# Kernel optimization log

Hardware: AMD Instinct MI355X
Metric: run time of the kernel (lower is better)

The kernel has to match this reference:

```python
import jax, jax.numpy as jnp
import numpy as np

# dims: V vocab, D embed, C classes, S seq, L layers, M proj_dim (random features), B batch
V, D, C, S, L, M, B = 32000, 512, 2, 2048, 4, 64, 16
H = 4 * D  # FFN hidden


def setup_inputs() -> dict:
    key = jax.random.key(0)
    ks = jax.random.split(key, 16)
    sc = 0.02
    n = lambda k, shape, s=sc: jax.random.normal(k, shape, jnp.float32) * s
    return {
        'x': jax.random.randint(ks[0], (B, S), 0, V),
        'embed': n(ks[1], (V, D)),
        'pos': n(ks[2], (S, D)),
        'Wq': n(ks[3], (L, D, D)), 'bq': jnp.zeros((L, D), jnp.float32),
        'Wk': n(ks[4], (L, D, D)), 'bk': jnp.zeros((L, D), jnp.float32),
        'Wv': n(ks[5], (L, D, D)), 'bv': jnp.zeros((L, D), jnp.float32),
        'P': jax.random.normal(ks[6], (L, D, M), jnp.float32) / np.sqrt(D),  # Performer random-feature projection
        'Wo': n(ks[7], (L, D, D)), 'bo': jnp.zeros((L, D), jnp.float32),
        'ln_g': jnp.ones((L, D), jnp.float32), 'ln_b': jnp.zeros((L, D), jnp.float32),
        'W1': n(ks[8], (L, D, H)), 'b1': jnp.zeros((L, H), jnp.float32),
        'W2': n(ks[9], (L, H, D)), 'b2': jnp.zeros((L, D), jnp.float32),
        'Wc1': n(ks[10], (D, D // 2)), 'bc1': jnp.zeros((D // 2,), jnp.float32),
        'Wc2': n(ks[11], (D // 2, C)), 'bc2': jnp.zeros((C,), jnp.float32),
    }


def _layernorm(x, g, b, eps=1e-5):
    mu = x.mean(-1, keepdims=True)
    var = ((x - mu) ** 2).mean(-1, keepdims=True)
    return (x - mu) * jax.lax.rsqrt(var + eps) * g + b


def reference(x, embed, pos, Wq, bq, Wk, bk, Wv, bv, P, Wo, bo,
              ln_g, ln_b, W1, b1, W2, b2, Wc1, bc1, Wc2, bc2):
    # token embedding + learned positional embedding
    h = embed[x] + pos[None, :, :]  # [B,S,D]
    for l in range(L):
        r = h
        # Performer linear attention
        q = h @ Wq[l] + bq[l]
        k = h @ Wk[l] + bk[l]
        v = h @ Wv[l] + bv[l]
        pq = jax.nn.elu(q @ P[l]) + 1.0  # [B,S,M] positive feature map
        pk = jax.nn.elu(k @ P[l]) + 1.0
        kv = jnp.einsum('bsm,bsd->bmd', pk, v)              # associative K^T V reduction
        z = jnp.einsum('bsm,bm->bs', pq, pk.sum(axis=1)) + 1e-6
        att = jnp.einsum('bsm,bmd->bsd', pq, kv) / z[..., None]
        att = att @ Wo[l] + bo[l]
        # LayerNorm -> FFN (dropout is identity in eval)
        hn = _layernorm(att, ln_g[l], ln_b[l])
        ff = jax.nn.gelu(hn @ W1[l] + b1[l], approximate=False) @ W2[l] + b2[l]
        h = ff + r  # residual around the whole Sequential block
    pooled = h[:, 0, :]  # CLS pooling
    hid = jax.nn.relu(pooled @ Wc1 + bc1)
    return hid @ Wc2 + bc2  # [B,C] logits
```

## Files before the change

kernel.cpp:

```cpp
#include <hip/hip_runtime.h>
#include <hip/hip_bf16.h>
#include <math.h>

constexpr int kV = 32000;
constexpr int kD = 512;
constexpr int kC = 2;
constexpr int kS = 2048;
constexpr int kL = 4;
constexpr int kM = 64;
constexpr int kB = 16;
constexpr int kH = 2048;
constexpr int kBS = kB * kS;

typedef __hip_bfloat16 bf16;
using bf16x8 = __attribute__((ext_vector_type(8))) short;
using f32x4  = __attribute__((ext_vector_type(4))) float;

#define GLOBAL_LOAD_LDS16(gp, lp)                                              \
  __builtin_amdgcn_global_load_lds(                                            \
      (const __attribute__((address_space(1))) void*)(gp),                     \
      (__attribute__((address_space(3))) void*)(lp), 16, 0, 0)

__device__ inline unsigned short f2bf_u16(float f) {
  bf16 b = __float2bfloat16(f);
  return *reinterpret_cast<unsigned short*>(&b);
}

__global__ __launch_bounds__(256) void embed_kernel(const int* __restrict__ x,
    const float* __restrict__ emb, const float* __restrict__ pos,
    float* __restrict__ h, bf16* __restrict__ hb) {
  int tid = blockIdx.x * 256 + threadIdx.x;
  int row = tid >> 7;
  int d4  = tid & 127;
  int tok = x[row];
  int s   = row & (kS - 1);
  float4 e = ((const float4*)emb)[(size_t)tok * 128 + d4];
  float4 p = ((const float4*)pos)[(size_t)s * 128 + d4];
  float4 o;
  o.x = e.x + p.x; o.y = e.y + p.y; o.z = e.z + p.z; o.w = e.w + p.w;
  ((float4*)h)[(size_t)row * 128 + d4] = o;
  ushort4 ub;
  ub.x = f2bf_u16(o.x); ub.y = f2bf_u16(o.y);
  ub.z = f2bf_u16(o.z); ub.w = f2bf_u16(o.w);
  ((ushort4*)hb)[(size_t)row * 128 + d4] = ub;
}

__global__ __launch_bounds__(256) void transpose_cast_kernel(
    const float* __restrict__ W, bf16* __restrict__ Wt, int K, int N) {
  __shared__ float tile[32][33];
  const int k0 = blockIdx.x * 32, n0 = blockIdx.y * 32;
  int tx = threadIdx.x & 31, ty = threadIdx.x >> 5;
#pragma unroll
  for (int i = 0; i < 32; i += 8)
    tile[ty + i][tx] = W[(size_t)(k0 + ty + i) * N + n0 + tx];
  __syncthreads();
#pragma unroll
  for (int i = 0; i < 32; i += 8)
    Wt[(size_t)(n0 + ty + i) * K + k0 + tx] = __float2bfloat16(tile[tx][ty + i]);
}

__global__ __launch_bounds__(256) void cast_bf16_kernel(
    const float* __restrict__ src, bf16* __restrict__ dst) {
  int gid = blockIdx.x * 256 + threadIdx.x;
  float4 v = ((const float4*)src)[gid];
  ushort4 u;
  u.x = f2bf_u16(v.x); u.y = f2bf_u16(v.y);
  u.z = f2bf_u16(v.z); u.w = f2bf_u16(v.w);
  ((ushort4*)dst)[gid] = u;
}

__global__ __launch_bounds__(256) void zero512_kernel(float* __restrict__ p) {
  if (threadIdx.x < 128) ((float4*)p)[threadIdx.x] = make_float4(0.f, 0.f, 0.f, 0.f);
}

__global__ __launch_bounds__(256) void wfold_dual_kernel(
    const float* __restrict__ Wq, const float* __restrict__ Wk,
    const float* __restrict__ P, bf16* __restrict__ Wqpt,
    bf16* __restrict__ Wkpt) {
  int gid = blockIdx.x * 256 + threadIdx.x;
  const float* W = (gid < 32768) ? Wq : Wk;
  bf16* out      = (gid < 32768) ? Wqpt : Wkpt;
  int id = gid & 32767;
  int m  = id & 63;
  int kk = id >> 6;
  float a0 = 0.f, a1 = 0.f, a2 = 0.f, a3 = 0.f;
#pragma unroll 4
  for (int c = 0; c < kD; c += 4) {
    float4 w = *(const float4*)&W[(size_t)kk * kD + c];
    a0 = fmaf(w.x, P[(size_t)(c + 0) * kM + m], a0);
    a1 = fmaf(w.y, P[(size_t)(c + 1) * kM + m], a1);
    a2 = fmaf(w.z, P[(size_t)(c + 2) * kM + m], a2);
    a3 = fmaf(w.w, P[(size_t)(c + 3) * kM + m], a3);
  }
  out[(size_t)m * kD + kk] = __float2bfloat16((a0 + a1) + (a2 + a3));
}

__global__ __launch_bounds__(128) void bfold_kernel(const float* __restrict__ bq,
    const float* __restrict__ bk, const float* __restrict__ P,
    float* __restrict__ bqp, float* __restrict__ bkp) {
  int m = threadIdx.x & (kM - 1);
  const float* src = (threadIdx.x >> 6) ? bk : bq;
  float* dst = (threadIdx.x >> 6) ? bkp : bqp;
  float acc = 0.f;
  for (int c = 0; c < kD; ++c) acc += src[c] * P[(size_t)c * kM + m];
  dst[m] = acc;
}

__global__ __launch_bounds__(256) void bvwo_kernel(const float* __restrict__ bv,
    const float* __restrict__ Wo, float* __restrict__ bvWo) {
  __shared__ float part[4][64];
  int d0 = blockIdx.x * 64;
  int dc = threadIdx.x & 63;
  int eg = threadIdx.x >> 6;
  float acc = 0.f;
  int e0 = eg * 128;
#pragma unroll 4
  for (int e = e0; e < e0 + 128; ++e)
    acc = fmaf(bv[e], Wo[(size_t)e * kD + d0 + dc], acc);
  part[eg][dc] = acc;
  __syncthreads();
  if (eg == 0)
    bvWo[d0 + dc] = (part[0][dc] + part[1][dc]) + (part[2][dc] + part[3][dc]);
}

template <int BK, int BN, int ACT, bool HAS_RES, bool HAS_OUTER, bool WRITE_F32, bool WRITE_BF16>
__global__ __launch_bounds__(256) void mfma_gemm(
    const bf16* __restrict__ A, const bf16* __restrict__ Wt,
    const float* __restrict__ bias, const float* __restrict__ rowv,
    const float* __restrict__ colv, const float* __restrict__ res,
    float* __restrict__ C, bf16* __restrict__ Cb, int K, int N) {
  constexpr int NJ = BN / 32;
  constexpr int CPR = BK / 8;
  constexpr int SW = (BK == 32) ? 1 : 0;
  __shared__ short As[128 * BK];
  __shared__ short Bs[BN * BK];
  const int tid  = threadIdx.x;
  const int lane = tid & 63;
  const int wave = tid >> 6;
  const int nx = gridDim.x;
  const int SH = (gridDim.y & 7) ? gridDim.y : 8;
  const int b_lin = blockIdx.y * nx + blockIdx.x;
  const int stripe = b_lin / (nx * SH);
  const int rem = b_lin - stripe * (nx * SH);
  const int row0 = (stripe * SH + (rem % SH)) * 128;
  const int col0 = (rem / SH) * BN;
  const int wr = (wave & 1) * 64;
  const int wc = (wave >> 1) * (BN / 2);
  const int lcol = lane & 15;
  const int quad = lane >> 4;

  f32x4 acc[4][NJ];
#pragma unroll
  for (int i = 0; i < 4; ++i)
#pragma unroll
    for (int j = 0; j < NJ; ++j) acc[i][j] = (f32x4){0.f, 0.f, 0.f, 0.f};

  for (int k0 = 0; k0 < K; k0 += BK) {
#pragma unroll
    for (int p = 0; p < 128 * CPR / 256; ++p) {
      int idx = p * 256 + tid;
      int r = idx / CPR;
      int kc = (idx % CPR) ^ ((r >> SW) & (CPR - 1));
      GLOBAL_LOAD_LDS16(&A[(size_t)(row0 + r) * K + k0 + kc * 8], &As[idx * 8]);
    }
#pragma unroll
    for (int p = 0; p < BN * CPR / 256; ++p) {
      int idx = p * 256 + tid;
      int r = idx / CPR;
      int kc = (idx % CPR) ^ ((r >> SW) & (CPR - 1));
      GLOBAL_LOAD_LDS16(&Wt[(size_t)(col0 + r) * K + k0 + kc * 8], &Bs[idx * 8]);
    }
    __syncthreads();
#pragma unroll
    for (int kh = 0; kh < BK / 32; ++kh) {
      bf16x8 af[4], bfr[NJ];
#pragma unroll
      for (int i = 0; i < 4; ++i) {
        int rr = wr + i * 16 + lcol;
        int slot = (kh * 4 + quad) ^ ((rr >> SW) & (CPR - 1));
        af[i] = *(const bf16x8*)&As[(rr * CPR + slot) * 8];
      }
#pragma unroll
      for (int j = 0; j < NJ; ++j) {
        int rr = wc + j * 16 + lcol;
        int slot = (kh * 4 + quad) ^ ((rr >> SW) & (CPR - 1));
        bfr[j] = *(const bf16x8*)&Bs[(rr * CPR + slot) * 8];
      }
#pragma unroll
      for (int i = 0; i < 4; ++i)
#pragma unroll
        for (int j = 0; j < NJ; ++j)
          acc[i][j] = __builtin_amdgcn_mfma_f32_16x16x32_bf16(af[i], bfr[j], acc[i][j], 0, 0, 0);
    }
    __syncthreads();
  }

#pragma unroll
  for (int i = 0; i < 4; ++i) {
#pragma unroll
    for (int r = 0; r < 4; ++r) {
      int grow = row0 + wr + i * 16 + quad * 4 + r;
#pragma unroll
      for (int j = 0; j < NJ; ++j) {
        int gcol = col0 + wc + j * 16 + lcol;
        float v = acc[i][j][r];
        if (HAS_OUTER) v += rowv[grow] * colv[gcol];
        else v += bias[gcol];
        if (ACT == 2) v = 0.5f * v * (1.0f + erff(v * 0.70710678118654752f));
        size_t off = (size_t)grow * N + gcol;
        if (HAS_RES) v += res[off];
        if (WRITE_F32) C[off] = v;
        if (WRITE_BF16) Cb[off] = __float2bfloat16(v);
      }
    }
  }
}

template <int ACT, bool HAS_RES, bool WRITE_F32, bool WRITE_BF16>
__global__ __launch_bounds__(512) void mfma_gemm_256(
    const bf16* __restrict__ A, const bf16* __restrict__ Wt,
    const float* __restrict__ bias, const float* __restrict__ res,
    float* __restrict__ C, bf16* __restrict__ Cb, int K, int N) {
  constexpr int BK = 64, BN = 128, BM = 256;
  __shared__ short As[BM * BK];
  __shared__ short Bs[BN * BK];
  const int tid  = threadIdx.x;
  const int lane = tid & 63;
  const int wave = tid >> 6;
  const int nx = gridDim.x;
  const int SH = (gridDim.y & 7) ? gridDim.y : 8;
  const int b_lin = blockIdx.y * nx + blockIdx.x;
  const int stripe = b_lin / (nx * SH);
  const int rem = b_lin - stripe * (nx * SH);
  const int row0 = (stripe * SH + (rem % SH)) * BM;
  const int col0 = (rem / SH) * BN;
  const int wr = (wave & 3) * 64;
  const int wc = (wave >> 2) * 64;
  const int lcol = lane & 15;
  const int quad = lane >> 4;

  f32x4 acc[4][4];
#pragma unroll
  for (int i = 0; i < 4; ++i)
#pragma unroll
    for (int j = 0; j < 4; ++j) acc[i][j] = (f32x4){0.f, 0.f, 0.f, 0.f};

  for (int k0 = 0; k0 < K; k0 += BK) {
#pragma unroll
    for (int p = 0; p < 4; ++p) {
      int idx = p * 512 + tid;
      int r = idx >> 3;
      int kc = (idx & 7) ^ (r & 7);
      GLOBAL_LOAD_LDS16(&A[(size_t)(row0 + r) * K + k0 + kc * 8], &As[idx * 8]);
    }
#pragma unroll
    for (int p = 0; p < 2; ++p) {
      int idx = p * 512 + tid;
      int r = idx >> 3;
      int kc = (idx & 7) ^ (r & 7);
      GLOBAL_LOAD_LDS16(&Wt[(size_t)(col0 + r) * K + k0 + kc * 8], &Bs[idx * 8]);
    }
    __syncthreads();
#pragma unroll
    for (int kh = 0; kh < 2; ++kh) {
      bf16x8 af[4], bfr[4];
#pragma unroll
      for (int i = 0; i < 4; ++i) {
        int rr = wr + i * 16 + lcol;
        int slot = (kh * 4 + quad) ^ (rr & 7);
        af[i] = *(const bf16x8*)&As[(rr * 8 + slot) * 8];
      }
#pragma unroll
      for (int j = 0; j < 4; ++j) {
        int rr = wc + j * 16 + lcol;
        int slot = (kh * 4 + quad) ^ (rr & 7);
        bfr[j] = *(const bf16x8*)&Bs[(rr * 8 + slot) * 8];
      }
#pragma unroll
      for (int i = 0; i < 4; ++i)
#pragma unroll
        for (int j = 0; j < 4; ++j)
          acc[i][j] = __builtin_amdgcn_mfma_f32_16x16x32_bf16(af[i], bfr[j], acc[i][j], 0, 0, 0);
    }
    __syncthreads();
  }

#pragma unroll
  for (int i = 0; i < 4; ++i) {
#pragma unroll
    for (int r = 0; r < 4; ++r) {
      int grow = row0 + wr + i * 16 + quad * 4 + r;
#pragma unroll
      for (int j = 0; j < 4; ++j) {
        int gcol = col0 + wc + j * 16 + lcol;
        float v = acc[i][j][r] + bias[gcol];
        if (ACT == 2) v = 0.5f * v * (1.0f + erff(v * 0.70710678118654752f));
        size_t off = (size_t)grow * N + gcol;
        if (HAS_RES) v += res[off];
        if (WRITE_F32) C[off] = v;
        if (WRITE_BF16) Cb[off] = __float2bfloat16(v);
      }
    }
  }
}

__global__ __launch_bounds__(256) void skinny_dual_gemm(
    const bf16* __restrict__ A, const bf16* __restrict__ Wq,
    const bf16* __restrict__ Wk, const float* __restrict__ bq,
    const float* __restrict__ bk, float* __restrict__ pq,
    float* __restrict__ pk) {
  __shared__ short As[64 * 32];
  __shared__ short Bs[128 * 32];
  const int tid  = threadIdx.x;
  const int lane = tid & 63;
  const int wave = tid >> 6;
  const int row0 = blockIdx.x * 64;
  const int lcol = lane & 15;
  const int quad = lane >> 4;

  f32x4 accq[4], acck[4];
#pragma unroll
  for (int i = 0; i < 4; ++i) {
    accq[i] = (f32x4){0.f, 0.f, 0.f, 0.f};
    acck[i] = (f32x4){0.f, 0.f, 0.f, 0.f};
  }

  for (int k0 = 0; k0 < kD; k0 += 32) {
    {
      int r = tid >> 2;
      int kc = (tid & 3) ^ ((r >> 1) & 3);
      GLOBAL_LOAD_LDS16(&A[(size_t)(row0 + r) * kD + k0 + kc * 8], &As[tid * 8]);
    }
#pragma unroll
    for (int p = 0; p < 2; ++p) {
      int idx = p * 256 + tid;
      int r = idx >> 2;
      int kc = (idx & 3) ^ ((r >> 1) & 3);
      const bf16* src = (r < 64) ? &Wq[(size_t)r * kD + k0 + kc * 8]
                                 : &Wk[(size_t)(r - 64) * kD + k0 + kc * 8];
      GLOBAL_LOAD_LDS16(src, &Bs[idx * 8]);
    }
    __syncthreads();
    bf16x8 af[4], bq_f, bk_f;
#pragma unroll
    for (int i = 0; i < 4; ++i) {
      int rr = i * 16 + lcol;
      af[i] = *(const bf16x8*)&As[(rr * 4 + (quad ^ ((rr >> 1) & 3))) * 8];
    }
    {
      int rr = wave * 16 + lcol;
      bq_f = *(const bf16x8*)&Bs[(rr * 4 + (quad ^ ((rr >> 1) & 3))) * 8];
      int rr2 = 64 + wave * 16 + lcol;
      bk_f = *(const bf16x8*)&Bs[(rr2 * 4 + (quad ^ ((rr2 >> 1) & 3))) * 8];
    }
#pragma unroll
    for (int i = 0; i < 4; ++i) {
      accq[i] = __builtin_amdgcn_mfma_f32_16x16x32_bf16(af[i], bq_f, accq[i], 0, 0, 0);
      acck[i] = __builtin_amdgcn_mfma_f32_16x16x32_bf16(af[i], bk_f, acck[i], 0, 0, 0);
    }
    __syncthreads();
  }

#pragma unroll
  for (int i = 0; i < 4; ++i) {
#pragma unroll
    for (int r = 0; r < 4; ++r) {
      int grow = row0 + i * 16 + quad * 4 + r;
      int gcol = wave * 16 + lcol;
      float vq = accq[i][r] + bq[gcol];
      vq = (vq > 0.f) ? (vq + 1.f) : expf(vq);
      pq[(size_t)grow * kM + gcol] = vq;
      float vk = acck[i][r] + bk[gcol];
      vk = (vk > 0.f) ? (vk + 1.f) : expf(vk);
      pk[(size_t)grow * kM + gcol] = vk;
    }
  }
}

__global__ __launch_bounds__(256) void kvh_split_kernel(const float* __restrict__ pk,
    const bf16* __restrict__ hb, float* __restrict__ part) {
  __shared__ float pkS[16][64];
  __shared__ float vS[16][256];
  const int d0 = blockIdx.x * 256, b = blockIdx.y, split = blockIdx.z;
  const int s_beg = split * 128;
  const float* pkb = pk + (size_t)b * kS * kM;
  const bf16* hbb  = hb + (size_t)b * kS * kD;
  const int tid = threadIdx.x;
  const int tx = tid & 15, ty = tid >> 4;
  float4 acc[4][4];
#pragma unroll
  for (int i = 0; i < 4; ++i)
#pragma unroll
    for (int j = 0; j < 4; ++j) acc[i][j] = make_float4(0.f, 0.f, 0.f, 0.f);

  for (int s0 = s_beg; s0 < s_beg + 128; s0 += 16) {
    {
      int e = tid * 4;
      int sr = e >> 6, mc = e & 63;
      *(float4*)&pkS[sr][mc] = *(const float4*)&pkb[(size_t)(s0 + sr) * kM + mc];
    }
#pragma unroll
    for (int p = 0; p < 2; ++p) {
      int idx = p * 256 + tid;
      int sr = idx >> 5, dc8 = idx & 31;
      uint4 raw = *(const uint4*)&hbb[(size_t)(s0 + sr) * kD + d0 + dc8 * 8];
      float4 f0, f1;
      f0.x = __uint_as_float(raw.x << 16);
      f0.y = __uint_as_float(raw.x & 0xffff0000u);
      f0.z = __uint_as_float(raw.y << 16);
      f0.w = __uint_as_float(raw.y & 0xffff0000u);
      f1.x = __uint_as_float(raw.z << 16);
      f1.y = __uint_as_float(raw.z & 0xffff0000u);
      f1.z = __uint_as_float(raw.w << 16);
      f1.w = __uint_as_float(raw.w & 0xffff0000u);
      *(float4*)&vS[sr][dc8 * 8]     = f0;
      *(float4*)&vS[sr][dc8 * 8 + 4] = f1;
    }
    __syncthreads();
#pragma unroll
    for (int sr = 0; sr < 16; ++sr) {
      float a[4];
#pragma unroll
      for (int i = 0; i < 4; ++i) a[i] = pkS[sr][ty * 4 + i];
      float4 bv4[4];
#pragma unroll
      for (int j = 0; j < 4; ++j) bv4[j] = *(const float4*)&vS[sr][tx * 16 + j * 4];
#pragma unroll
      for (int i = 0; i < 4; ++i)
#pragma unroll
        for (int j = 0; j < 4; ++j) {
          acc[i][j].x += a[i] * bv4[j].x;
          acc[i][j].y += a[i] * bv4[j].y;
          acc[i][j].z += a[i] * bv4[j].z;
          acc[i][j].w += a[i] * bv4[j].w;
        }
    }
    __syncthreads();
  }
  float* pp = part + (((size_t)split * kB + b) * kM) * kD;
#pragma unroll
  for (int i = 0; i < 4; ++i)
#pragma unroll
    for (int j = 0; j < 4; ++j)
      *(float4*)&pp[(size_t)(ty * 4 + i) * kD + d0 + tx * 16 + j * 4] = acc[i][j];
}

__global__ __launch_bounds__(256) void kvh_reduce_kernel(const float* __restrict__ part,
                                                         bf16* __restrict__ kvhb) {
  int gid = blockIdx.x * 256 + threadIdx.x;
  float4 s = make_float4(0.f, 0.f, 0.f, 0.f);
#pragma unroll
  for (int sp = 0; sp < 16; ++sp) {
    float4 p = ((const float4*)part)[(size_t)sp * (kB * kM * kD / 4) + gid];
    s.x += p.x; s.y += p.y; s.z += p.z; s.w += p.w;
  }
  ushort4 u;
  u.x = f2bf_u16(s.x); u.y = f2bf_u16(s.y);
  u.z = f2bf_u16(s.z); u.w = f2bf_u16(s.w);
  ((ushort4*)kvhb)[gid] = u;
}

__global__ __launch_bounds__(256) void zero_pks_kernel(float* __restrict__ p) {
  ((float4*)p)[threadIdx.x] = make_float4(0.f, 0.f, 0.f, 0.f);
}

__global__ __launch_bounds__(256) void pksum_kernel(const float* __restrict__ pk,
                                                    float* __restrict__ pksum) {
  __shared__ float part[4][64];
  int b = blockIdx.x >> 4;
  int split = blockIdx.x & 15;
  int lane = threadIdx.x & 63, w = threadIdx.x >> 6;
  float s = 0.f;
  int base = split * 128 + w * 32;
  for (int i = 0; i < 32; ++i)
    s += pk[((size_t)b * kS + base + i) * kM + lane];
  part[w][lane] = s;
  __syncthreads();
  if (w == 0)
    atomicAdd(&pksum[b * kM + lane],
              part[0][lane] + part[1][lane] + part[2][lane] + part[3][lane]);
}

__global__ __launch_bounds__(256) void z_kernel(const float* __restrict__ pq,
    const float* __restrict__ pksum, float* __restrict__ z) {
  int row = blockIdx.x * 4 + (threadIdx.x >> 6);
  int lane = threadIdx.x & 63;
  int b = row >> 11;
  float v = pq[(size_t)row * kM + lane] * pksum[b * kM + lane];
#pragma unroll
  for (int off = 32; off; off >>= 1) v += __shfl_down(v, off);
  if (lane == 0) z[row] = v + 1e-6f;
}

__global__ __launch_bounds__(256) void att_ln_kernel(
    const float* __restrict__ pq, const float* __restrict__ kvo,
    const float* __restrict__ z, const float* __restrict__ bo,
    const float* __restrict__ g, const float* __restrict__ bb,
    bf16* __restrict__ out) {
  __shared__ float pqS[32][68];
  __shared__ float kvS[16][520];
  const int s0 = blockIdx.x * 32, b = blockIdx.y;
  const int tid = threadIdx.x;
  const int tx = tid & 15, ty = tid >> 4;

#pragma unroll
  for (int i = 0; i < 2; ++i) {
    int f4 = tid + i * 256;
    int r = f4 >> 4, c = (f4 & 15) * 4;
    *(float4*)&pqS[r][c] = *(const float4*)&pq[((size_t)(b * kS + s0 + r)) * kM + c];
  }

  float4 acc[2][8];
#pragma unroll
  for (int i = 0; i < 2; ++i)
#pragma unroll
    for (int j = 0; j < 8; ++j) acc[i][j] = make_float4(0.f, 0.f, 0.f, 0.f);

  for (int m0 = 0; m0 < kM; m0 += 16) {
#pragma unroll
    for (int p = 0; p < 8; ++p) {
      int idx = p * 256 + tid;
      int sr = idx >> 7, c4 = idx & 127;
      *(float4*)&kvS[sr][c4 * 4] =
          *(const float4*)&kvo[((size_t)b * kM + m0 + sr) * kD + c4 * 4];
    }
    __syncthreads();
#pragma unroll
    for (int mm = 0; mm < 16; ++mm) {
      float a0 = pqS[ty * 2 + 0][m0 + mm];
      float a1 = pqS[ty * 2 + 1][m0 + mm];
#pragma unroll
      for (int j = 0; j < 8; ++j) {
        float4 bv = *(const float4*)&kvS[mm][j * 64 + tx * 4];
        acc[0][j].x += a0 * bv.x; acc[0][j].y += a0 * bv.y;
        acc[0][j].z += a0 * bv.z; acc[0][j].w += a0 * bv.w;
        acc[1][j].x += a1 * bv.x; acc[1][j].y += a1 * bv.y;
        acc[1][j].z += a1 * bv.z; acc[1][j].w += a1 * bv.w;
      }
    }
    __syncthreads();
  }

  float zi0 = 1.0f / z[b * kS + s0 + ty * 2 + 0];
  float zi1 = 1.0f / z[b * kS + s0 + ty * 2 + 1];
#pragma unroll
  for (int j = 0; j < 8; ++j) {
    float4 bo4 = *(const float4*)&bo[j * 64 + tx * 4];
    acc[0][j].x = acc[0][j].x * zi0 + bo4.x; acc[0][j].y = acc[0][j].y * zi0 + bo4.y;
    acc[0][j].z = acc[0][j].z * zi0 + bo4.z; acc[0][j].w = acc[0][j].w * zi0 + bo4.w;
    acc[1][j].x = acc[1][j].x * zi1 + bo4.x; acc[1][j].y = acc[1][j].y * zi1 + bo4.y;
    acc[1][j].z = acc[1][j].z * zi1 + bo4.z; acc[1][j].w = acc[1][j].w * zi1 + bo4.w;
  }

#pragma unroll
  for (int i = 0; i < 2; ++i) {
    float s = 0.f;
#pragma unroll
    for (int j = 0; j < 8; ++j)
      s += (acc[i][j].x + acc[i][j].y) + (acc[i][j].z + acc[i][j].w);
    s += __shfl_xor(s, 1); s += __shfl_xor(s, 2);
    s += __shfl_xor(s, 4); s += __shfl_xor(s, 8);
    float mean = s * (1.0f / kD);
    float v2 = 0.f;
#pragma unroll
    for (int j = 0; j < 8; ++j) {
      float dx = acc[i][j].x - mean, dy = acc[i][j].y - mean;
      float dz = acc[i][j].z - mean, dw = acc[i][j].w - mean;
      v2 += (dx * dx + dy * dy) + (dz * dz + dw * dw);
    }
    v2 += __shfl_xor(v2, 1); v2 += __shfl_xor(v2, 2);
    v2 += __shfl_xor(v2, 4); v2 += __shfl_xor(v2, 8);
    float rstd = rsqrtf(v2 * (1.0f / kD) + 1e-5f);
    size_t rowoff = ((size_t)(b * kS + s0 + ty * 2 + i)) * kD;
#pragma unroll
    for (int j = 0; j < 8; ++j) {
      int col = j * 64 + tx * 4;
      float4 g4 = *(const float4*)&g[col];
      float4 b4 = *(const float4*)&bb[col];
      ushort4 u;
      u.x = f2bf_u16((acc[i][j].x - mean) * rstd * g4.x + b4.x);
      u.y = f2bf_u16((acc[i][j].y - mean) * rstd * g4.y + b4.y);
      u.z = f2bf_u16((acc[i][j].z - mean) * rstd * g4.z + b4.z);
      u.w = f2bf_u16((acc[i][j].w - mean) * rstd * g4.w + b4.w);
      *(ushort4*)&out[rowoff + col] = u;
    }
  }
}

__global__ __launch_bounds__(256) void cls_kernel(const float* __restrict__ h,
    const float* __restrict__ Wc1, const float* __restrict__ bc1,
    const float* __restrict__ Wc2, const float* __restrict__ bc2,
    float* __restrict__ out) {
  __shared__ float r0[4], r1[4];
  int b = blockIdx.x;
  int j = threadIdx.x;
  const float* p = h + (size_t)b * kS * kD;
  float acc = bc1[j];
  for (int i = 0; i < kD; ++i) acc += p[i] * Wc1[i * (kD / 2) + j];
  acc = fmaxf(acc, 0.f);
  float p0 = acc * Wc2[j * kC + 0];
  float p1 = acc * Wc2[j * kC + 1];
#pragma unroll
  for (int off = 32; off; off >>= 1) {
    p0 += __shfl_down(p0, off);
    p1 += __shfl_down(p1, off);
  }
  if ((j & 63) == 0) { r0[j >> 6] = p0; r1[j >> 6] = p1; }
  __syncthreads();
  if (j == 0) {
    out[b * kC + 0] = r0[0] + r0[1] + r0[2] + r0[3] + bc2[0];
    out[b * kC + 1] = r1[0] + r1[1] + r1[2] + r1[3] + bc2[1];
  }
}

extern "C" void kernel_launch(void* const* d_in, const int* in_sizes, int n_in,
                              void* d_out, int out_size, void* d_ws, size_t ws_size,
                              hipStream_t stream) {
  const int*   x    = (const int*)  d_in[0];
  const float* emb  = (const float*)d_in[1];
  const float* pos  = (const float*)d_in[2];
  const float* Wq   = (const float*)d_in[3];
  const float* bq   = (const float*)d_in[4];
  const float* Wk   = (const float*)d_in[5];
  const float* bk   = (const float*)d_in[6];
  const float* Wv   = (const float*)d_in[7];
  const float* bv   = (const float*)d_in[8];
  const float* P    = (const float*)d_in[9];
  const float* Wo   = (const float*)d_in[10];
  const float* bo   = (const float*)d_in[11];
  const float* ln_g = (const float*)d_in[12];
  const float* ln_b = (const float*)d_in[13];
  const float* W1   = (const float*)d_in[14];
  const float* b1   = (const float*)d_in[15];
  const float* W2   = (const float*)d_in[16];
  const float* b2   = (const float*)d_in[17];
  const float* Wc1  = (const float*)d_in[18];
  const float* bc1  = (const float*)d_in[19];
  const float* Wc2  = (const float*)d_in[20];
  const float* bc2  = (const float*)d_in[21];
  float* out = (float*)d_out;

  float* h    = (float*)d_ws;
  float* t0   = h    + (size_t)kBS * kD;
  float* pq   = t0   + (size_t)kBS * kD;
  float* pk   = pq   + (size_t)kBS * kM;
  float* kvo  = pk   + (size_t)kBS * kM;
  float* pks  = kvo  + (size_t)kB * kM * kD;
  float* zb   = pks  + (size_t)kB * kM;
  float* bqp  = zb   + kBS;
  float* bkp  = bqp  + kM;
  float* bvWo = bkp  + kM;
  float* zeros= bvWo + kD;
  bf16* hb    = (bf16*)(zeros + kD);
  bf16* ab    = hb + (size_t)kBS * kD;
  bf16* Wqpt  = ab  + (size_t)kBS * kD;
  bf16* Wkpt  = Wqpt + (size_t)kM * kD;
  bf16* Wot   = Wkpt + (size_t)kM * kD;
  bf16* Wvc   = Wot + (size_t)kD * kD;
  bf16* WvWot = Wvc + (size_t)kD * kD;
  bf16* W1t   = WvWot + (size_t)kD * kD;
  bf16* W2t   = W1t + (size_t)kD * kH;
  bf16* kvhb  = W2t + (size_t)kD * kH;
  bf16* F     = (bf16*)t0;
  float* kvpart = (float*)ab;

  zero512_kernel<<<1, 256, 0, stream>>>(zeros);
  embed_kernel<<<kBS * (kD / 4) / 256, 256, 0, stream>>>(x, emb, pos, h, hb);

  for (int l = 0; l < kL; ++l) {
    const float* Pl = P + (size_t)l * kD * kM;

    wfold_dual_kernel<<<256, 256, 0, stream>>>(
        Wq + (size_t)l * kD * kD, Wk + (size_t)l * kD * kD, Pl, Wqpt, Wkpt);
    bfold_kernel<<<1, 128, 0, stream>>>(bq + l * kD, bk + l * kD, Pl, bqp, bkp);
    transpose_cast_kernel<<<dim3(kD / 32, kD / 32), 256, 0, stream>>>(
        Wo + (size_t)l * kD * kD, Wot, kD, kD);
    cast_bf16_kernel<<<kD * kD / 1024, 256, 0, stream>>>(Wv + (size_t)l * kD * kD, Wvc);
    mfma_gemm<32, 64, 0, false, false, false, true><<<dim3(8, 4), 256, 0, stream>>>(
        Wot, Wvc, zeros, nullptr, nullptr, nullptr, nullptr, WvWot, kD, kD);
    bvwo_kernel<<<8, 256, 0, stream>>>(bv + l * kD, Wo + (size_t)l * kD * kD, bvWo);
    transpose_cast_kernel<<<dim3(kD / 32, kH / 32), 256, 0, stream>>>(
        W1 + (size_t)l * kD * kH, W1t, kD, kH);
    transpose_cast_kernel<<<dim3(kH / 32, kD / 32), 256, 0, stream>>>(
        W2 + (size_t)l * kH * kD, W2t, kH, kD);

    skinny_dual_gemm<<<kBS / 64, 256, 0, stream>>>(hb, Wqpt, Wkpt, bqp, bkp, pq, pk);
    kvh_split_kernel<<<dim3(kD / 256, kB, 16), 256, 0, stream>>>(pk, hb, kvpart);
    kvh_reduce_kernel<<<kB * kM * kD / 1024, 256, 0, stream>>>(kvpart, kvhb);
    zero_pks_kernel<<<1, 256, 0, stream>>>(pks);
    pksum_kernel<<<kB * 16, 256, 0, stream>>>(pk, pks);
    z_kernel<<<kBS / 4, 256, 0, stream>>>(pq, pks, zb);
    mfma_gemm<32, 64, 0, false, true, true, false><<<dim3(8, 8), 256, 0, stream>>>(
        kvhb, WvWot, nullptr, pks, bvWo, nullptr, kvo, nullptr, kD, kD);
    att_ln_kernel<<<dim3(kS / 32, kB), 256, 0, stream>>>(
        pq, kvo, zb, bo + l * kD, ln_g + l * kD, ln_b + l * kD, ab);
    for (int c = 0; c < 2; ++c) {
      size_t ro = (size_t)c * 16384;
      mfma_gemm_256<2, false, false, true><<<dim3(kH / 128, 16384 / 256), 512, 0, stream>>>(
          ab + ro * kD, W1t, b1 + l * kH, nullptr, nullptr, F, kD, kH);
      mfma_gemm_256<0, true, true, true><<<dim3(kD / 128, 16384 / 256), 512, 0, stream>>>(
          F, W2t, b2 + l * kD, h + ro * kD, h + ro * kD, hb + ro * kD, kH, kD);
    }
  }

  cls_kernel<<<kB, 256, 0, stream>>>(h, Wc1, bc1, Wc2, bc2, out);
}
```

Measured before the change: 1.789 ms.

## Double-buffer LDS in FFN GEMM with smaller 128x128 tiles

Rewrites the FFN GEMM kernel to use two LDS buffers so the global-to-LDS loads for the next K tile are issued before computing the current one, with one barrier per iteration instead of two. The block tile shrinks from 256x128 to 128x128, each wave now computing 64x32, and the grid doubles in the M direction. This aims to hide memory latency and raise occupancy, at the cost of less data reuse per block and fewer MFMAs per LDS read.

```diff
diff --git a/kernel.cpp b/kernel.cpp
--- a/kernel.cpp
+++ b/kernel.cpp
@@ -217,13 +217,13 @@
 }
 
 template <int ACT, bool HAS_RES, bool WRITE_F32, bool WRITE_BF16>
-__global__ __launch_bounds__(512) void mfma_gemm_256(
+__global__ __launch_bounds__(512) void mfma_gemm_2ph(
     const bf16* __restrict__ A, const bf16* __restrict__ Wt,
     const float* __restrict__ bias, const float* __restrict__ res,
     float* __restrict__ C, bf16* __restrict__ Cb, int K, int N) {
-  constexpr int BK = 64, BN = 128, BM = 256;
-  __shared__ short As[BM * BK];
-  __shared__ short Bs[BN * BK];
+  constexpr int BK = 64, BN = 128, BM = 128;
+  __shared__ short As[2][BM * BK];
+  __shared__ short Bs[2][BN * BK];
   const int tid  = threadIdx.x;
   const int lane = tid & 63;
   const int wave = tid >> 6;
@@ -234,55 +234,71 @@
   const int rem = b_lin - stripe * (nx * SH);
   const int row0 = (stripe * SH + (rem % SH)) * BM;
   const int col0 = (rem / SH) * BN;
-  const int wr = (wave & 3) * 64;
-  const int wc = (wave >> 2) * 64;
+  const int wr = (wave & 1) * 64;
+  const int wc = (wave >> 1) * 32;
   const int lcol = lane & 15;
   const int quad = lane >> 4;
 
-  f32x4 acc[4][4];
+  f32x4 acc[4][2];
 #pragma unroll
   for (int i = 0; i < 4; ++i)
 #pragma unroll
-    for (int j = 0; j < 4; ++j) acc[i][j] = (f32x4){0.f, 0.f, 0.f, 0.f};
-
-  for (int k0 = 0; k0 < K; k0 += BK) {
-#pragma unroll
-    for (int p = 0; p < 4; ++p) {
-      int idx = p * 512 + tid;
-      int r = idx >> 3;
-      int kc = (idx & 7) ^ (r & 7);
-      GLOBAL_LOAD_LDS16(&A[(size_t)(row0 + r) * K + k0 + kc * 8], &As[idx * 8]);
-    }
+    for (int j = 0; j < 2; ++j) acc[i][j] = (f32x4){0.f, 0.f, 0.f, 0.f};
+
+  auto stage = [&](int buf, int k0) {
 #pragma unroll
     for (int p = 0; p < 2; ++p) {
       int idx = p * 512 + tid;
       int r = idx >> 3;
       int kc = (idx & 7) ^ (r & 7);
-      GLOBAL_LOAD_LDS16(&Wt[(size_t)(col0 + r) * K + k0 + kc * 8], &Bs[idx * 8]);
-    }
-    __syncthreads();
+      GLOBAL_LOAD_LDS16(&A[(size_t)(row0 + r) * K + k0 + kc * 8], &As[buf][idx * 8]);
+    }
+#pragma unroll
+    for (int p = 0; p < 2; ++p) {
+      int idx = p * 512 + tid;
+      int r = idx >> 3;
+      int kc = (idx & 7) ^ (r & 7);
+      GLOBAL_LOAD_LDS16(&Wt[(size_t)(col0 + r) * K + k0 + kc * 8], &Bs[buf][idx * 8]);
+    }
+  };
+
+  auto compute = [&](int buf) {
 #pragma unroll
     for (int kh = 0; kh < 2; ++kh) {
-      bf16x8 af[4], bfr[4];
+      bf16x8 af[4], bfr[2];
 #pragma unroll
       for (int i = 0; i < 4; ++i) {
         int rr = wr + i * 16 + lcol;
         int slot = (kh * 4 + quad) ^ (rr & 7);
-        af[i] = *(const bf16x8*)&As[(rr * 8 + slot) * 8];
+        af[i] = *(const bf16x8*)&As[buf][(rr * 8 + slot) * 8];
       }
 #pragma unroll
-      for (int j = 0; j < 4; ++j) {
+      for (int j = 0; j < 2; ++j) {
         int rr = wc + j * 16 + lcol;
         int slot = (kh * 4 + quad) ^ (rr & 7);
-        bfr[j] = *(const bf16x8*)&Bs[(rr * 8 + slot) * 8];
+        bfr[j] = *(const bf16x8*)&Bs[buf][(rr * 8 + slot) * 8];
       }
 #pragma unroll
       for (int i = 0; i < 4; ++i)
 #pragma unroll
-        for (int j = 0; j < 4; ++j)
+        for (int j = 0; j < 2; ++j)
           acc[i][j] = __builtin_amdgcn_mfma_f32_16x16x32_bf16(af[i], bfr[j], acc[i][j], 0, 0, 0);
     }
-    __syncthreads();
+  };
+
+  stage(0, 0);
+  asm volatile("s_waitcnt vmcnt(0)" ::: "memory");
+  __builtin_amdgcn_s_barrier();
+
+  const int NT = K / BK;
+  for (int t = 0; t < NT; ++t) {
+    const int cur = t & 1;
+    if (t + 1 < NT) stage(cur ^ 1, (t + 1) * BK);
+    compute(cur);
+    if (t + 1 < NT) {
+      asm volatile("s_waitcnt vmcnt(0)" ::: "memory");
+      __builtin_amdgcn_s_barrier();
+    }
   }
 
 #pragma unroll
@@ -291,7 +307,7 @@
     for (int r = 0; r < 4; ++r) {
       int grow = row0 + wr + i * 16 + quad * 4 + r;
 #pragma unroll
-      for (int j = 0; j < 4; ++j) {
+      for (int j = 0; j < 2; ++j) {
         int gcol = col0 + wc + j * 16 + lcol;
         float v = acc[i][j][r] + bias[gcol];
         if (ACT == 2) v = 0.5f * v * (1.0f + erff(v * 0.70710678118654752f));
@@ -696,9 +712,9 @@
         pq, kvo, zb, bo + l * kD, ln_g + l * kD, ln_b + l * kD, ab);
     for (int c = 0; c < 2; ++c) {
       size_t ro = (size_t)c * 16384;
-      mfma_gemm_256<2, false, false, true><<<dim3(kH / 128, 16384 / 256), 512, 0, stream>>>(
+      mfma_gemm_2ph<2, false, false, true><<<dim3(kH / 128, 16384 / 128), 512, 0, stream>>>(
           ab + ro * kD, W1t, b1 + l * kH, nullptr, nullptr, F, kD, kH);
-      mfma_gemm_256<0, true, true, true><<<dim3(kD / 128, 16384 / 256), 512, 0, stream>>>(
+      mfma_gemm_2ph<0, true, true, true><<<dim3(kD / 128, 16384 / 128), 512, 0, stream>>>(
           F, W2t, b2 + l * kD, h + ro * kD, h + ro * kD, hb + ro * kD, kH, kD);
     }
   }
```

After: 1.736 ms. -3.0%, faster.
